# Kernel tuning notes

Hardware: AMD Instinct MI355X
Metric: run time of the kernel (lower is better)

The kernel has to match this reference:

```python
import jax, jax.numpy as jnp
import numpy as np

TOP_K = 6  # num_experts_per_tok


def setup_inputs() -> dict:
    key = jax.random.key(0)
    k1, k2, k3, k4, k5 = jax.random.split(key, 5)
    B, S, H = 2, 2048, 2048
    E, M = 28, 1408
    scale = 0.02
    return {
        "hidden_states": jax.random.normal(k1, (B, S, H), jnp.float32),
        "gate_weight": jax.random.normal(k2, (E, H), jnp.float32) * scale,
        "w_gate": jax.random.normal(k3, (E, H, M), jnp.float32) * scale,
        "w_up": jax.random.normal(k4, (E, H, M), jnp.float32) * scale,
        "w_down": jax.random.normal(k5, (E, M, H), jnp.float32) * scale,
    }


def reference(hidden_states, gate_weight, w_gate, w_up, w_down):
    """DeepseekMoE forward (inference path): top-k softmax gating + expert
    dispatch/combine. gate_weight: [E, H]; w_gate/w_up: [E, H, M]; w_down: [E, M, H]."""
    B, S, H = hidden_states.shape
    x = hidden_states.reshape(-1, H)          # [T, H]
    T = x.shape[0]
    E = gate_weight.shape[0]

    # --- MoEGate: softmax scores, top-k, normalize top-k probs ---
    logits = x @ gate_weight.T                # [T, E]
    scores = jax.nn.softmax(logits, axis=-1)
    topk_w, topk_idx = jax.lax.top_k(scores, TOP_K)  # [T, K]
    topk_w = topk_w / (topk_w.sum(axis=-1, keepdims=True) + 1e-20)

    # Dense per-(token, expert) combine weights (0 for non-selected experts).
    cw = jnp.zeros((T, E), x.dtype).at[jnp.arange(T)[:, None], topk_idx].add(topk_w)

    # --- Expert compute + combine, scanning over experts to bound memory ---
    def step(y, inp):
        wg, wu, wd, w_tok = inp               # [H,M], [H,M], [M,H], [T]
        h = jax.nn.silu(x @ wg) * (x @ wu)    # [T, M]
        return y + w_tok[:, None] * (h @ wd), None

    y0 = jnp.zeros_like(x)
    y, _ = jax.lax.scan(step, y0, (w_gate, w_up, w_down, cw.T))
    return y.reshape(B, S, H)
```

## Files before the change

### kernel.cpp

```cpp
#include <hip/hip_runtime.h>
#include <stdint.h>

#define T_TOK 4096
#define HDIM 2048
#define MDIM 1408
#define NEXP 28
#define TOPK 6
#define NPAIR (T_TOK*TOPK)

typedef unsigned short u16;
typedef short short8 __attribute__((ext_vector_type(8)));
typedef float f32x4 __attribute__((ext_vector_type(4)));

__device__ __forceinline__ u16 f2bf(float x){
  unsigned int u = __float_as_uint(x);
  u += 0x7fffu + ((u >> 16) & 1u);
  return (u16)(u >> 16);
}
__device__ __forceinline__ float bf2f(unsigned int h){
  return __uint_as_float(h << 16);
}

__device__ __forceinline__ void gload16(const u16* g, u16* l){
  __builtin_amdgcn_global_load_lds((const __attribute__((address_space(1))) unsigned int*)g,
                                   (__attribute__((address_space(3))) unsigned int*)l,
                                   16, 0, 0);
}

__global__ __launch_bounds__(256) void cvt_kernel(const float* __restrict__ x,
                                                  u16* __restrict__ xb, int n8){
  int i = blockIdx.x*256 + threadIdx.x;
  if (i >= n8) return;
  const float4* s = (const float4*)x + (size_t)i*2;
  float4 a = s[0], b = s[1];
  unsigned int w0 = (unsigned)f2bf(a.x) | ((unsigned)f2bf(a.y)<<16);
  unsigned int w1 = (unsigned)f2bf(a.z) | ((unsigned)f2bf(a.w)<<16);
  unsigned int w2 = (unsigned)f2bf(b.x) | ((unsigned)f2bf(b.y)<<16);
  unsigned int w3 = (unsigned)f2bf(b.z) | ((unsigned)f2bf(b.w)<<16);
  uint4 o = {w0,w1,w2,w3};
  ((uint4*)xb)[i] = o;
}

__global__ __launch_bounds__(256) void transpose_cvt(const float* __restrict__ in,
                                                     u16* __restrict__ out, int K, int N){
  const int e = blockIdx.z;
  const int n0 = blockIdx.x*64, k0 = blockIdx.y*64;
  const float* src = in + ((size_t)e*K + k0)*N + n0;
  u16* dst = out + ((size_t)e*N + n0)*K + k0;
  __shared__ u16 td[64][65];
  const int tid = threadIdx.x;
  const int rk = tid>>4, rn = (tid&15)*4;
  #pragma unroll
  for (int i=0;i<4;i++){
    int k = rk + 16*i;
    float4 v = *(const float4*)(src + (size_t)k*N + rn);
    td[k][rn+0]=f2bf(v.x); td[k][rn+1]=f2bf(v.y);
    td[k][rn+2]=f2bf(v.z); td[k][rn+3]=f2bf(v.w);
  }
  __syncthreads();
  const int k8 = (tid&7)*8;
  #pragma unroll
  for (int i=0;i<2;i++){
    int n = (tid>>3) + 32*i;
    unsigned int w[4];
    #pragma unroll
    for (int j=0;j<4;j++)
      w[j] = (unsigned)td[k8+2*j][n] | ((unsigned)td[k8+2*j+1][n]<<16);
    uint4 o = {w[0],w[1],w[2],w[3]};
    *(uint4*)(dst + (size_t)n*K + k8) = o;
  }
}

__global__ __launch_bounds__(256) void gate_kernel(const float* __restrict__ x,
                                                   const float* __restrict__ gw,
                                                   int* __restrict__ topk_idx,
                                                   float* __restrict__ topk_w,
                                                   int* __restrict__ counts){
  const int wave = threadIdx.x >> 6, lane = threadIdx.x & 63;
  const int t = blockIdx.x*4 + wave;
  const float* xr = x + (size_t)t*HDIM;
  float xv[32];
  #pragma unroll
  for (int i=0;i<32;i++) xv[i] = xr[lane + 64*i];
  float sc[NEXP];
  #pragma unroll
  for (int e=0;e<NEXP;e++){
    const float* g = gw + (size_t)e*HDIM + lane;
    float a = 0.f;
    #pragma unroll
    for (int i=0;i<32;i++) a += xv[i]*g[64*i];
    #pragma unroll
    for (int d=32; d>0; d>>=1) a += __shfl_xor(a, d);
    sc[e] = a;
  }
  float mx = sc[0];
  #pragma unroll
  for (int e=1;e<NEXP;e++) mx = fmaxf(mx, sc[e]);
  unsigned int mask=0; int bi[TOPK]; float bs[TOPK]; float bsum=0.f;
  #pragma unroll
  for (int k=0;k<TOPK;k++){
    float bm=-3.4e38f; int bj=0;
    #pragma unroll
    for (int e=0;e<NEXP;e++){
      bool ok = (((mask>>e)&1u)==0u) && (sc[e]>bm);
      bm = ok ? sc[e] : bm; bj = ok ? e : bj;
    }
    mask |= (1u<<bj);
    float s = expf(bm - mx);
    bi[k]=bj; bs[k]=s; bsum+=s;
  }
  if (lane==0){
    float inv = 1.f/(bsum + 1e-20f);
    #pragma unroll
    for (int k=0;k<TOPK;k++){
      topk_idx[t*TOPK+k]=bi[k];
      topk_w[t*TOPK+k]=bs[k]*inv;
      atomicAdd(&counts[bi[k]],1);
    }
  }
}

__global__ void scan_kernel(const int* __restrict__ counts, int* __restrict__ offsets,
                            int* __restrict__ cursor){
  int t = threadIdx.x;
  if (t < NEXP) cursor[t] = 0;
  if (t == 0){
    int s = 0;
    for (int e=0;e<NEXP;e++){ offsets[e]=s; s+=counts[e]; }
    offsets[NEXP]=s;
  }
}

__global__ __launch_bounds__(256) void fill_kernel(const int* __restrict__ topk_idx,
                                                   const float* __restrict__ topk_w,
                                                   const int* __restrict__ offsets,
                                                   int* __restrict__ cursor,
                                                   int* __restrict__ pair_token,
                                                   int* __restrict__ pos){
  int t = blockIdx.x*256 + threadIdx.x;
  if (t >= T_TOK) return;
  #pragma unroll
  for (int k=0;k<TOPK;k++){
    int e = topk_idx[t*TOPK+k];
    int c = atomicAdd(&cursor[e],1);
    int p = offsets[e]+c;
    pair_token[p]=t;
    pos[t*TOPK+k]=p;
  }
}

template<int NB, bool GATHER, int EPI, int NBN>
__global__ __launch_bounds__(512,2) void gemm6(
    const u16* __restrict__ Ab, const u16* __restrict__ B0, const u16* __restrict__ B1,
    u16* __restrict__ Hout,
    const int* __restrict__ counts, const int* __restrict__ offsets,
    const int* __restrict__ pair_token,
    int K, int N, int cpx)
{
  extern __shared__ u16 smem[];
  constexpr int BUFSZ = (NB==2) ? 32768 : 24576;

  const int bid = blockIdx.x;
  const int swz = (bid & 7)*cpx + (bid >> 3);
  const int rb  = swz & 7;
  const int rest = swz >> 3;
  const int n0b = rest % NBN;
  const int e   = rest / NBN;

  const int cnt = counts[e];
  const int row0 = rb*256;
  if (row0 >= cnt) return;
  const int off = offsets[e];
  const int n0 = n0b*128;

  const int tid = threadIdx.x;
  const int lane = tid&63, wid = tid>>6;
  const int wm = wid>>2, wn = wid&3;
  const int lrow = lane&15, lgrp = lane>>4;

  const u16* ap[4]; const u16* bp0[2]; const u16* bp1[2];
  #pragma unroll
  for (int i=0;i<4;i++){
    int c = tid + 512*i;
    int r = c>>3;
    int u = (c&7) ^ (r&7);
    int pr = off + min(row0 + r, cnt-1);
    const u16* arow = GATHER ? (Ab + (size_t)pair_token[pr]*K) : (Ab + (size_t)pr*K);
    ap[i] = arow + u*8;
  }
  #pragma unroll
  for (int i=0;i<2;i++){
    int c = tid + 512*i;
    int r = c>>3;
    int u = (c&7) ^ (r&7);
    size_t brow = (size_t)e*N + (size_t)(n0 + r);
    bp0[i] = B0 + brow*K + u*8;
    if (NB==2) bp1[i] = B1 + brow*K + u*8;
  }

  const int sA0 = ((lgrp)     ^ (lrow&7))*8;
  const int sA1 = ((4+lgrp)   ^ (lrow&7))*8;
  const int abase = (wm*128 + lrow)*64;
  const int bbase = 16384 + (wn*32 + lrow)*64;

  f32x4 acc0[8][2] = {};
  f32x4 acc1[8][2] = {};

  const int nt = K/64;

  #pragma unroll
  for (int i=0;i<4;i++) gload16(ap[i], &smem[(tid+512*i)*8]);
  #pragma unroll
  for (int i=0;i<2;i++){
    gload16(bp0[i], &smem[16384 + (tid+512*i)*8]);
    if (NB==2) gload16(bp1[i], &smem[24576 + (tid+512*i)*8]);
  }
  #pragma unroll
  for (int i=0;i<4;i++) gload16(ap[i] + 64, &smem[BUFSZ + (tid+512*i)*8]);
  #pragma unroll
  for (int i=0;i<2;i++){
    gload16(bp0[i] + 64, &smem[BUFSZ + 16384 + (tid+512*i)*8]);
    if (NB==2) gload16(bp1[i] + 64, &smem[BUFSZ + 24576 + (tid+512*i)*8]);
  }
  if (NB==2) asm volatile("s_waitcnt vmcnt(8)" ::: "memory");
  else       asm volatile("s_waitcnt vmcnt(6)" ::: "memory");
  __builtin_amdgcn_s_barrier();

  for (int t=0; t<nt; ++t){
    const u16* sc = smem + (t&1)*BUFSZ;
    u16* sn = (u16*)sc;

    short8 af[2][8], b0f[2][2], b1f[2][2];
    #pragma unroll
    for (int fm=0;fm<8;fm++){
      af[0][fm] = *(const short8*)&sc[abase + fm*1024 + sA0];
      af[1][fm] = *(const short8*)&sc[abase + fm*1024 + sA1];
    }
    #pragma unroll
    for (int fn=0;fn<2;fn++){
      b0f[0][fn] = *(const short8*)&sc[bbase + fn*1024 + sA0];
      b0f[1][fn] = *(const short8*)&sc[bbase + fn*1024 + sA1];
      if (NB==2){
        b1f[0][fn] = *(const short8*)&sc[8192 + bbase + fn*1024 + sA0];
        b1f[1][fn] = *(const short8*)&sc[8192 + bbase + fn*1024 + sA1];
      }
    }
    asm volatile("s_waitcnt lgkmcnt(0)" ::: "memory");
    __builtin_amdgcn_sched_barrier(0);
    __builtin_amdgcn_s_barrier();

    if (t+2 < nt){
      const int kt = (t+2)*64;
      #pragma unroll
      for (int i=0;i<4;i++) gload16(ap[i] + kt, &sn[(tid+512*i)*8]);
      #pragma unroll
      for (int i=0;i<2;i++){
        gload16(bp0[i] + kt, &sn[16384 + (tid+512*i)*8]);
        if (NB==2) gload16(bp1[i] + kt, &sn[24576 + (tid+512*i)*8]);
      }
    }
    __builtin_amdgcn_sched_barrier(0);

    __builtin_amdgcn_s_setprio(1);
    #pragma unroll
    for (int kh=0;kh<2;kh++){
      #pragma unroll
      for (int fm=0;fm<8;fm++){
        #pragma unroll
        for (int fn=0;fn<2;fn++){
          acc0[fm][fn] = __builtin_amdgcn_mfma_f32_16x16x32_bf16(af[kh][fm], b0f[kh][fn], acc0[fm][fn],0,0,0);
          if (NB==2)
            acc1[fm][fn] = __builtin_amdgcn_mfma_f32_16x16x32_bf16(af[kh][fm], b1f[kh][fn], acc1[fm][fn],0,0,0);
        }
      }
    }
    __builtin_amdgcn_s_setprio(0);

    if (t+1 < nt){
      if (t+2 < nt){
        if (NB==2) asm volatile("s_waitcnt vmcnt(8)" ::: "memory");
        else       asm volatile("s_waitcnt vmcnt(6)" ::: "memory");
      } else {
        asm volatile("s_waitcnt vmcnt(0)" ::: "memory");
      }
      __builtin_amdgcn_s_barrier();
    }
  }

  #pragma unroll
  for (int fm=0;fm<8;fm++){
    #pragma unroll
    for (int j=0;j<4;j++){
      int grow = wm*128 + fm*16 + lgrp*4 + j;
      if (row0+grow < cnt){
        int p = off + row0 + grow;
        u16* hrow = Hout + (size_t)p*N;
        #pragma unroll
        for (int fn=0;fn<2;fn++){
          int col = n0 + wn*32 + fn*16 + lrow;
          if (EPI==0){
            float g = acc0[fm][fn][j], u = acc1[fm][fn][j];
            hrow[col] = f2bf(g*u/(1.f+expf(-g)));
          } else {
            hrow[col] = f2bf(acc0[fm][fn][j]);
          }
        }
      }
    }
  }
}

__global__ __launch_bounds__(256) void combine_kernel(const u16* __restrict__ pairbuf,
                                                      const int* __restrict__ pos,
                                                      const float* __restrict__ topk_w,
                                                      float* __restrict__ out){
  const int t = blockIdx.x;
  const int c = threadIdx.x*8;
  float acc[8] = {};
  #pragma unroll
  for (int k=0;k<TOPK;k++){
    int p = pos[t*TOPK+k];
    float w = topk_w[t*TOPK+k];
    uint4 v = *(const uint4*)&pairbuf[(size_t)p*HDIM + c];
    unsigned int ws_[4] = {v.x,v.y,v.z,v.w};
    #pragma unroll
    for (int j=0;j<4;j++){
      acc[2*j]   += w*bf2f(ws_[j]&0xffffu);
      acc[2*j+1] += w*bf2f(ws_[j]>>16);
    }
  }
  float4 o0 = {acc[0],acc[1],acc[2],acc[3]};
  float4 o1 = {acc[4],acc[5],acc[6],acc[7]};
  float* orow = out + (size_t)t*HDIM + c;
  *(float4*)orow = o0;
  *(float4*)(orow+4) = o1;
}

extern "C" void kernel_launch(void* const* d_in, const int* in_sizes, int n_in,
                              void* d_out, int out_size, void* d_ws, size_t ws_size,
                              hipStream_t stream) {
  const float* x  = (const float*)d_in[0];
  const float* gw = (const float*)d_in[1];
  const float* wg = (const float*)d_in[2];
  const float* wu = (const float*)d_in[3];
  const float* wd = (const float*)d_in[4];
  float* out = (float*)d_out;

  const size_t WT_BYTES = (size_t)NEXP*MDIM*HDIM*2;

  char* p = (char*)d_ws;
  u16* wg_t = (u16*)p;
  u16* wd_t = (u16*)p;
  p += WT_BYTES;
  u16* wu_t    = (u16*)p;
  u16* pairbuf = (u16*)p;
  p += WT_BYTES;
  u16* xb   = (u16*)p; p += (size_t)T_TOK*HDIM*2;
  u16* hbuf = (u16*)p; p += (size_t)NPAIR*MDIM*2;
  int*   topk_idx   = (int*)p;   p += NPAIR*4;
  float* topk_w     = (float*)p; p += NPAIR*4;
  int*   pair_token = (int*)p;   p += NPAIR*4;
  int*   pos        = (int*)p;   p += NPAIR*4;
  int*   counts     = (int*)p;   p += 128;
  int*   offsets    = (int*)p;   p += 128;
  int*   cursor     = (int*)p;   p += 128;

  hipMemsetAsync(counts, 0, 128, stream);
  cvt_kernel<<<T_TOK*HDIM/8/256, 256, 0, stream>>>(x, xb, T_TOK*HDIM/8);
  gate_kernel<<<T_TOK/4, 256, 0, stream>>>(x, gw, topk_idx, topk_w, counts);
  scan_kernel<<<1, 64, 0, stream>>>(counts, offsets, cursor);
  fill_kernel<<<T_TOK/256, 256, 0, stream>>>(topk_idx, topk_w, offsets, cursor, pair_token, pos);

  transpose_cvt<<<dim3(MDIM/64, HDIM/64, NEXP), 256, 0, stream>>>(wg, wg_t, HDIM, MDIM);
  transpose_cvt<<<dim3(MDIM/64, HDIM/64, NEXP), 256, 0, stream>>>(wu, wu_t, HDIM, MDIM);

  {
    int ntile = 8*(MDIM/128)*NEXP;
    gemm6<2,true,0,(MDIM/128)><<<ntile, 512, 131072, stream>>>(
        xb, wg_t, wu_t, hbuf, counts, offsets, pair_token, HDIM, MDIM, ntile/8);
  }

  transpose_cvt<<<dim3(HDIM/64, MDIM/64, NEXP), 256, 0, stream>>>(wd, wd_t, MDIM, HDIM);

  {
    int ntile = 8*(HDIM/128)*NEXP;
    gemm6<1,false,1,(HDIM/128)><<<ntile, 512, 98304, stream>>>(
        hbuf, wd_t, nullptr, pairbuf, counts, offsets, pair_token, MDIM, HDIM, ntile/8);
  }

  combine_kernel<<<T_TOK, 256, 0, stream>>>(pairbuf, pos, topk_w, out);
}
```

Baseline: 1.056 ms.

## Use 4x2 warp layout with 64x64 warp tiles and reorder prefetch after MFMA

Changes the per-warp tile from 128x32 to 64x64 (4x2 warps instead of 2x4), which cuts LDS fragment reads per MFMA by balancing A and B reuse. It moves the next-tile global prefetch and the barrier to after the MFMA block, with LDS reads interleaved under raised priority. Launch bounds drop to one block per CU, allowing more registers but lowering occupancy.

```diff
diff --git a/kernel.cpp b/kernel.cpp
--- a/kernel.cpp
+++ b/kernel.cpp
@@ -26,6 +26,8 @@
                                    (__attribute__((address_space(3))) unsigned int*)l,
                                    16, 0, 0);
 }
+
+#define BAR_FENCE asm volatile("s_barrier" ::: "memory")
 
 __global__ __launch_bounds__(256) void cvt_kernel(const float* __restrict__ x,
                                                   u16* __restrict__ xb, int n8){
@@ -150,7 +152,7 @@
 }
 
 template<int NB, bool GATHER, int EPI, int NBN>
-__global__ __launch_bounds__(512,2) void gemm6(
+__global__ __launch_bounds__(512,1) void gemm8(
     const u16* __restrict__ Ab, const u16* __restrict__ B0, const u16* __restrict__ B1,
     u16* __restrict__ Hout,
     const int* __restrict__ counts, const int* __restrict__ offsets,
@@ -175,7 +177,7 @@
 
   const int tid = threadIdx.x;
   const int lane = tid&63, wid = tid>>6;
-  const int wm = wid>>2, wn = wid&3;
+  const int wm = wid>>1, wn = wid&1;
   const int lrow = lane&15, lgrp = lane>>4;
 
   const u16* ap[4]; const u16* bp0[2]; const u16* bp1[2];
@@ -198,13 +200,13 @@
     if (NB==2) bp1[i] = B1 + brow*K + u*8;
   }
 
-  const int sA0 = ((lgrp)     ^ (lrow&7))*8;
-  const int sA1 = ((4+lgrp)   ^ (lrow&7))*8;
-  const int abase = (wm*128 + lrow)*64;
-  const int bbase = 16384 + (wn*32 + lrow)*64;
-
-  f32x4 acc0[8][2] = {};
-  f32x4 acc1[8][2] = {};
+  const int sA0 = ((lgrp)   ^ (lrow&7))*8;
+  const int sA1 = ((4+lgrp) ^ (lrow&7))*8;
+  const int abase = (wm*64 + lrow)*64;
+  const int bbase = 16384 + (wn*64 + lrow)*64;
+
+  f32x4 acc0[4][4] = {};
+  f32x4 acc1[4][4] = {};
 
   const int nt = K/64;
 
@@ -224,50 +226,31 @@
   }
   if (NB==2) asm volatile("s_waitcnt vmcnt(8)" ::: "memory");
   else       asm volatile("s_waitcnt vmcnt(6)" ::: "memory");
-  __builtin_amdgcn_s_barrier();
+  BAR_FENCE;
 
   for (int t=0; t<nt; ++t){
     const u16* sc = smem + (t&1)*BUFSZ;
     u16* sn = (u16*)sc;
 
-    short8 af[2][8], b0f[2][2], b1f[2][2];
-    #pragma unroll
-    for (int fm=0;fm<8;fm++){
-      af[0][fm] = *(const short8*)&sc[abase + fm*1024 + sA0];
-      af[1][fm] = *(const short8*)&sc[abase + fm*1024 + sA1];
-    }
-    #pragma unroll
-    for (int fn=0;fn<2;fn++){
-      b0f[0][fn] = *(const short8*)&sc[bbase + fn*1024 + sA0];
-      b0f[1][fn] = *(const short8*)&sc[bbase + fn*1024 + sA1];
-      if (NB==2){
-        b1f[0][fn] = *(const short8*)&sc[8192 + bbase + fn*1024 + sA0];
-        b1f[1][fn] = *(const short8*)&sc[8192 + bbase + fn*1024 + sA1];
+    short8 af[2][4], b0f[2][4], b1f[2][4];
+    __builtin_amdgcn_s_setprio(1);
+    #pragma unroll
+    for (int kh=0;kh<2;kh++){
+      const int sk = kh ? sA1 : sA0;
+      #pragma unroll
+      for (int fm=0;fm<4;fm++) af[kh][fm] = *(const short8*)&sc[abase + fm*1024 + sk];
+      #pragma unroll
+      for (int fn=0;fn<4;fn++){
+        b0f[kh][fn] = *(const short8*)&sc[bbase + fn*1024 + sk];
+        if (NB==2) b1f[kh][fn] = *(const short8*)&sc[8192 + bbase + fn*1024 + sk];
       }
     }
-    asm volatile("s_waitcnt lgkmcnt(0)" ::: "memory");
-    __builtin_amdgcn_sched_barrier(0);
-    __builtin_amdgcn_s_barrier();
-
-    if (t+2 < nt){
-      const int kt = (t+2)*64;
-      #pragma unroll
-      for (int i=0;i<4;i++) gload16(ap[i] + kt, &sn[(tid+512*i)*8]);
-      #pragma unroll
-      for (int i=0;i<2;i++){
-        gload16(bp0[i] + kt, &sn[16384 + (tid+512*i)*8]);
-        if (NB==2) gload16(bp1[i] + kt, &sn[24576 + (tid+512*i)*8]);
-      }
-    }
-    __builtin_amdgcn_sched_barrier(0);
-
-    __builtin_amdgcn_s_setprio(1);
     #pragma unroll
     for (int kh=0;kh<2;kh++){
       #pragma unroll
-      for (int fm=0;fm<8;fm++){
+      for (int fm=0;fm<4;fm++){
         #pragma unroll
-        for (int fn=0;fn<2;fn++){
+        for (int fn=0;fn<4;fn++){
           acc0[fm][fn] = __builtin_amdgcn_mfma_f32_16x16x32_bf16(af[kh][fm], b0f[kh][fn], acc0[fm][fn],0,0,0);
           if (NB==2)
             acc1[fm][fn] = __builtin_amdgcn_mfma_f32_16x16x32_bf16(af[kh][fm], b1f[kh][fn], acc1[fm][fn],0,0,0);
@@ -276,28 +259,37 @@
     }
     __builtin_amdgcn_s_setprio(0);
 
-    if (t+1 < nt){
-      if (t+2 < nt){
-        if (NB==2) asm volatile("s_waitcnt vmcnt(8)" ::: "memory");
-        else       asm volatile("s_waitcnt vmcnt(6)" ::: "memory");
-      } else {
-        asm volatile("s_waitcnt vmcnt(0)" ::: "memory");
+    asm volatile("s_waitcnt lgkmcnt(0)" ::: "memory");
+    BAR_FENCE;
+
+    if (t+2 < nt){
+      const int kt = (t+2)*64;
+      #pragma unroll
+      for (int i=0;i<4;i++) gload16(ap[i] + kt, &sn[(tid+512*i)*8]);
+      #pragma unroll
+      for (int i=0;i<2;i++){
+        gload16(bp0[i] + kt, &sn[16384 + (tid+512*i)*8]);
+        if (NB==2) gload16(bp1[i] + kt, &sn[24576 + (tid+512*i)*8]);
       }
-      __builtin_amdgcn_s_barrier();
-    }
-  }
-
-  #pragma unroll
-  for (int fm=0;fm<8;fm++){
+      if (NB==2) asm volatile("s_waitcnt vmcnt(8)" ::: "memory");
+      else       asm volatile("s_waitcnt vmcnt(6)" ::: "memory");
+    } else if (t+1 < nt){
+      asm volatile("s_waitcnt vmcnt(0)" ::: "memory");
+    }
+    if (t+1 < nt) BAR_FENCE;
+  }
+
+  #pragma unroll
+  for (int fm=0;fm<4;fm++){
     #pragma unroll
     for (int j=0;j<4;j++){
-      int grow = wm*128 + fm*16 + lgrp*4 + j;
+      int grow = wm*64 + fm*16 + lgrp*4 + j;
       if (row0+grow < cnt){
         int p = off + row0 + grow;
         u16* hrow = Hout + (size_t)p*N;
         #pragma unroll
-        for (int fn=0;fn<2;fn++){
-          int col = n0 + wn*32 + fn*16 + lrow;
+        for (int fn=0;fn<4;fn++){
+          int col = n0 + wn*64 + fn*16 + lrow;
           if (EPI==0){
             float g = acc0[fm][fn][j], u = acc1[fm][fn][j];
             hrow[col] = f2bf(g*u/(1.f+expf(-g)));
@@ -376,7 +368,7 @@
 
   {
     int ntile = 8*(MDIM/128)*NEXP;
-    gemm6<2,true,0,(MDIM/128)><<<ntile, 512, 131072, stream>>>(
+    gemm8<2,true,0,(MDIM/128)><<<ntile, 512, 131072, stream>>>(
         xb, wg_t, wu_t, hbuf, counts, offsets, pair_token, HDIM, MDIM, ntile/8);
   }
 
@@ -384,7 +376,7 @@
 
   {
     int ntile = 8*(HDIM/128)*NEXP;
-    gemm6<1,false,1,(HDIM/128)><<<ntile, 512, 98304, stream>>>(
+    gemm8<1,false,1,(HDIM/128)><<<ntile, 512, 98304, stream>>>(
         hbuf, wd_t, nullptr, pairbuf, counts, offsets, pair_token, MDIM, HDIM, ntile/8);
   }
 
```

Result: no change. 1.065 ms (+0.9%).
